# Performance work log

Measured on AMD Instinct MI355X. Metric: run time of the kernel, lower is better.

The kernel has to match this reference:

```python
import jax, jax.numpy as jnp
import numpy as np

N_USER = 100000
N_ITEM = 50000
N = N_USER + N_ITEM
EMB = 64
FEAT = 384
NNZ = 2400000
N_PROMPT = 8
N_LAYERS = 4
EPS = 1e-8


def setup_inputs() -> dict:
    key = jax.random.key(0)
    ks = jax.random.split(key, 8)
    user_fea = jax.random.normal(ks[0], (N_USER, EMB), jnp.float32)
    item_fea = jax.random.normal(ks[1], (N_ITEM, FEAT), jnp.float32)
    prompt_embedding = jax.random.normal(ks[2], (N_PROMPT, EMB), jnp.float32)
    mlp_w = jax.random.normal(ks[3], (FEAT, EMB), jnp.float32) / np.sqrt(FEAT)
    mlp_b = jnp.zeros((EMB,), jnp.float32)
    adj_rows = jax.random.randint(ks[4], (NNZ,), 0, N, jnp.int32)
    adj_cols = jax.random.randint(ks[5], (NNZ,), 0, N, jnp.int32)
    # normalized-adjacency-like positive values
    adj_vals = jax.random.uniform(ks[6], (NNZ,), jnp.float32) * 0.01
    return dict(user_fea=user_fea, item_fea=item_fea,
                prompt_embedding=prompt_embedding, mlp_w=mlp_w, mlp_b=mlp_b,
                adj_rows=adj_rows, adj_cols=adj_cols, adj_vals=adj_vals)


def _spmm(rows, cols, vals, x):
    # sparse [N,N] @ dense [N,E] via gather + segment-sum
    return jax.ops.segment_sum(vals[:, None] * x[cols], rows, num_segments=N)


def reference(user_fea, item_fea, prompt_embedding, mlp_w, mlp_b,
              adj_rows, adj_cols, adj_vals):
    prompt_embd = jnp.sum(prompt_embedding, axis=0)            # [EMB]
    user_embd = user_fea + prompt_embd[None, :]                # [N_USER, EMB]
    item_embd = jnp.tanh(item_fea @ mlp_w + mlp_b)             # [N_ITEM, EMB]
    ego = jnp.concatenate([user_embd, item_embd], axis=0)      # [N, EMB]
    ego_norm = jnp.linalg.norm(ego, axis=-1)                   # [N]

    x = ego
    acc = ego  # running sum over layer stack (layer 0 = ego)
    for _ in range(N_LAYERS):
        x = _spmm(adj_rows, adj_cols, adj_vals, x)
        # cosine similarity of propagated embedding vs ego embedding, per row
        denom = jnp.maximum(jnp.linalg.norm(x, axis=-1) * ego_norm, EPS)
        w = jnp.sum(x * ego, axis=-1) / denom                  # [N]
        x = w[:, None] * x
        acc = acc + x

    return acc[:N_USER], acc[N_USER:]
```

## Files before the change

kernel.cpp:

```cpp
#include <hip/hip_runtime.h>
#include <hip/hip_fp16.h>

constexpr int kNUser = 100000;
constexpr int kNItem = 50000;
constexpr int kN     = 150000;
constexpr int kEmb   = 64;
constexpr int kFeat  = 384;
constexpr int kNnz   = 2400000;
constexpr float kEps = 1e-8f;

constexpr int kChunk = 1024;
constexpr int kNB    = (kN + kChunk - 1) / kChunk;

constexpr int kNBkt   = 256;
constexpr int kBR     = (kN + kNBkt - 1) / kNBkt;
constexpr int kChunkA = 4096;
constexpr int kNWGA   = (kNnz + kChunkA - 1) / kChunkA;

constexpr int kKS     = kFeat / 32;
constexpr int kNT     = kEmb / 16;
constexpr int kWElems = kKS * kNT * 64 * 8;

typedef __attribute__((ext_vector_type(8))) short short8v;
typedef __attribute__((ext_vector_type(4))) float floatx4;

__device__ inline unsigned short f2bf(float f) {
    unsigned u = __float_as_uint(f);
    return (unsigned short)((u + 0x7FFFu + ((u >> 16) & 1u)) >> 16);
}
__device__ inline float bf2f(unsigned short h) {
    return __uint_as_float((unsigned)h << 16);
}


__global__ void prompt_sum_k(const float* __restrict__ p, float* __restrict__ out) {
    int d = threadIdx.x;
    float s = 0.f;
#pragma unroll
    for (int i = 0; i < 8; ++i) s += p[i * kEmb + d];
    out[d] = s;
}

__global__ void user_ego_k(const float* __restrict__ uf, const float* __restrict__ ps,
                           float* __restrict__ ego) {
    int i = blockIdx.x * blockDim.x + threadIdx.x;
    if (i >= kNUser * kEmb) return;
    ego[i] = uf[i] + ps[i & 63];
}

__global__ void wsplit_k(const float* __restrict__ w, unsigned short* __restrict__ whi,
                         unsigned short* __restrict__ wlo) {
    int t = blockIdx.x * 256 + threadIdx.x;
    if (t >= kWElems) return;
    int j    = t & 7;
    int lane = (t >> 3) & 63;
    int nt   = (t >> 9) & 3;
    int ks   = t >> 11;
    int k = ks * 32 + (lane >> 4) * 8 + j;
    int n = nt * 16 + (lane & 15);
    float v = w[k * kEmb + n];
    unsigned short h = f2bf(v);
    whi[t] = h;
    wlo[t] = f2bf(v - bf2f(h));
}

__global__ __launch_bounds__(256)
void item_ego_mfma_k(const float* __restrict__ itf, const unsigned short* __restrict__ whi,
                     const unsigned short* __restrict__ wlo, const float* __restrict__ b,
                     float* __restrict__ ego) {
    int t    = threadIdx.x;
    int wid  = t >> 6;
    int lane = t & 63;
    int r0   = blockIdx.x * 64 + wid * 16;
    int arow = r0 + (lane & 15);
    int kg   = lane >> 4;
    bool av  = arow < kNItem;
    const float* ap = itf + (size_t)(av ? arow : 0) * kFeat + kg * 8;

    const short8v* whv = (const short8v*)whi;
    const short8v* wlv = (const short8v*)wlo;

    floatx4 accH[kNT], accL[kNT];
#pragma unroll
    for (int nt = 0; nt < kNT; ++nt) {
        accH[nt] = (floatx4){0.f, 0.f, 0.f, 0.f};
        accL[nt] = (floatx4){0.f, 0.f, 0.f, 0.f};
    }

    for (int ks = 0; ks < kKS; ++ks) {
        const float4 z = make_float4(0.f, 0.f, 0.f, 0.f);
        float4 a0 = av ? *(const float4*)(ap + ks * 32)     : z;
        float4 a1 = av ? *(const float4*)(ap + ks * 32 + 4) : z;
        short8v ah, al;
#pragma unroll
        for (int j = 0; j < 8; ++j) {
            float f = (j < 4) ? ((const float*)&a0)[j] : ((const float*)&a1)[j - 4];
            unsigned short h = f2bf(f);
            ah[j] = (short)h;
            al[j] = (short)f2bf(f - bf2f(h));
        }
#pragma unroll
        for (int nt = 0; nt < kNT; ++nt) {
            short8v bh = whv[(ks * kNT + nt) * 64 + lane];
            short8v bl = wlv[(ks * kNT + nt) * 64 + lane];
            accH[nt] = __builtin_amdgcn_mfma_f32_16x16x32_bf16(ah, bh, accH[nt], 0, 0, 0);
            accL[nt] = __builtin_amdgcn_mfma_f32_16x16x32_bf16(ah, bl, accL[nt], 0, 0, 0);
            accL[nt] = __builtin_amdgcn_mfma_f32_16x16x32_bf16(al, bh, accL[nt], 0, 0, 0);
        }
    }

    int col0  = lane & 15;
    int rsub  = (lane >> 4) * 4;
#pragma unroll
    for (int nt = 0; nt < kNT; ++nt) {
        float bb = b[nt * 16 + col0];
#pragma unroll
        for (int r = 0; r < 4; ++r) {
            int row = r0 + rsub + r;
            if (row < kNItem)
                ego[(size_t)(kNUser + row) * kEmb + nt * 16 + col0] =
                    tanhf(accH[nt][r] + accL[nt][r] + bb);
        }
    }
}

constexpr int kRW      = 16;
constexpr int kRowsBlk = 64;
constexpr int kKc      = 32;

__global__ __launch_bounds__(256, 2)
void item_ego_k(const float* __restrict__ itf, const float* __restrict__ w,
                const float* __restrict__ b, float* __restrict__ ego) {
    __shared__ float lds_a[kRowsBlk * kKc];
    int t      = threadIdx.x;
    int wid    = t >> 6;
    int lane   = t & 63;
    int blk_r0 = blockIdx.x * kRowsBlk;

    float acc[kRW];
#pragma unroll
    for (int r = 0; r < kRW; ++r) acc[r] = 0.f;

    int srow = t >> 3;
    int scol = (t & 7) * 4;

    for (int kc = 0; kc < kFeat; kc += kKc) {
        __syncthreads();
        {
            const float4 z = make_float4(0.f, 0.f, 0.f, 0.f);
            int gr0 = blk_r0 + srow;
            int gr1 = gr0 + 32;
            float4 v0 = (gr0 < kNItem)
                ? *(const float4*)(itf + (size_t)gr0 * kFeat + kc + scol) : z;
            float4 v1 = (gr1 < kNItem)
                ? *(const float4*)(itf + (size_t)gr1 * kFeat + kc + scol) : z;
            *(float4*)(lds_a + srow * kKc + scol)        = v0;
            *(float4*)(lds_a + (srow + 32) * kKc + scol) = v1;
        }
        float wreg[kKc];
#pragma unroll
        for (int k = 0; k < kKc; ++k) wreg[k] = w[(kc + k) * kEmb + lane];
        __syncthreads();
#pragma unroll
        for (int r = 0; r < kRW; ++r) {
            const float4* av = (const float4*)(lds_a + (wid * kRW + r) * kKc);
#pragma unroll
            for (int q = 0; q < 8; ++q) {
                float4 a = av[q];
                acc[r] = fmaf(a.x, wreg[q * 4 + 0], acc[r]);
                acc[r] = fmaf(a.y, wreg[q * 4 + 1], acc[r]);
                acc[r] = fmaf(a.z, wreg[q * 4 + 2], acc[r]);
                acc[r] = fmaf(a.w, wreg[q * 4 + 3], acc[r]);
            }
        }
    }
    float bv = b[lane];
#pragma unroll
    for (int r = 0; r < kRW; ++r) {
        int row = blk_r0 + wid * kRW + r;
        if (row < kNItem)
            ego[(size_t)(kNUser + row) * kEmb + lane] = tanhf(acc[r] + bv);
    }
}

__global__ void norm_init_csr_k(const float* __restrict__ ego, float* __restrict__ nrm,
                                float* __restrict__ acc, unsigned short* __restrict__ egoh) {
    int wid  = threadIdx.x >> 6;
    int lane = threadIdx.x & 63;
    int row  = blockIdx.x * 4 + wid;
    if (row >= kN) return;
    size_t idx = (size_t)row * kEmb + lane;
    float e = ego[idx];
    acc[idx] = e;
    __half h = __float2half_rn(e);
    egoh[idx] = *(unsigned short*)&h;
    float s = e * e;
#pragma unroll
    for (int o = 32; o >= 1; o >>= 1) s += __shfl_xor(s, o, 64);
    if (lane == 0) nrm[row] = sqrtf(s);
}


__global__ void hist_k(const int* __restrict__ rows, int* __restrict__ cnt) {
    int e = blockIdx.x * blockDim.x + threadIdx.x;
    if (e < kNnz) atomicAdd(&cnt[rows[e]], 1);
}

__global__ void scan1_k(const int* __restrict__ cnt, int* __restrict__ excl_out,
                        int* __restrict__ blk_sum) {
    __shared__ int sd[256];
    int b = blockIdx.x, t = threadIdx.x;
    int base = b * kChunk + t * 4;
    int c0 = (base + 0 < kN) ? cnt[base + 0] : 0;
    int c1 = (base + 1 < kN) ? cnt[base + 1] : 0;
    int c2 = (base + 2 < kN) ? cnt[base + 2] : 0;
    int c3 = (base + 3 < kN) ? cnt[base + 3] : 0;
    int tsum = c0 + c1 + c2 + c3;
    sd[t] = tsum;
    __syncthreads();
#pragma unroll
    for (int off = 1; off < 256; off <<= 1) {
        int v = (t >= off) ? sd[t - off] : 0;
        __syncthreads();
        sd[t] += v;
        __syncthreads();
    }
    int excl = sd[t] - tsum;
    if (t == 255) blk_sum[b] = sd[255];
    int run = excl;
    if (base + 0 < kN) { excl_out[base + 0] = run; run += c0; }
    if (base + 1 < kN) { excl_out[base + 1] = run; run += c1; }
    if (base + 2 < kN) { excl_out[base + 2] = run; run += c2; }
    if (base + 3 < kN) { excl_out[base + 3] = run; run += c3; }
}

__global__ void scan2_k(const int* __restrict__ blk_sum, int* __restrict__ blk_off) {
    __shared__ int sd[256];
    int t = threadIdx.x;
    int v = (t < kNB) ? blk_sum[t] : 0;
    sd[t] = v;
    __syncthreads();
#pragma unroll
    for (int off = 1; off < 256; off <<= 1) {
        int u = (t >= off) ? sd[t - off] : 0;
        __syncthreads();
        sd[t] += u;
        __syncthreads();
    }
    if (t < kNB) blk_off[t] = sd[t] - v;
}

__global__ void scan3_k(int* __restrict__ rp, int* __restrict__ rf,
                        const int* __restrict__ blk_off) {
    int b = blockIdx.x, t = threadIdx.x;
    int base = b * kChunk + t * 4;
    int o = blk_off[b];
#pragma unroll
    for (int k = 0; k < 4; ++k) {
        int i = base + k;
        if (i < kN) { int v = rp[i] + o; rp[i] = v; rf[i] = v; }
    }
    if (b == 0 && t == 0) rp[kN] = kNnz;
}

__global__ void bbase_k(const int* __restrict__ rp, int* __restrict__ bbase) {
    int b = blockIdx.x * blockDim.x + threadIdx.x;
    if (b <= kNBkt) {
        int r = b * kBR;
        bbase[b] = rp[r < kN ? r : kN];
    }
}

__global__ __launch_bounds__(256)
void bucket_k(const int* __restrict__ rows, const int* __restrict__ cols,
              const float* __restrict__ vals, const int* __restrict__ bbase,
              int* __restrict__ bfill, int2* __restrict__ tmp) {
    __shared__ int cnt[kNBkt];
    __shared__ int wgbase[kNBkt];
    int t  = threadIdx.x;
    int e0 = blockIdx.x * kChunkA;
    for (int i = t; i < kNBkt; i += 256) cnt[i] = 0;
    __syncthreads();
    int myb[kChunkA / 256];
    int myoff[kChunkA / 256];
#pragma unroll
    for (int k = 0; k < kChunkA / 256; ++k) {
        int e = e0 + k * 256 + t;
        if (e < kNnz) {
            int b = rows[e] / kBR;
            myb[k]   = b;
            myoff[k] = atomicAdd(&cnt[b], 1);
        } else {
            myb[k] = -1;
        }
    }
    __syncthreads();
    for (int i = t; i < kNBkt; i += 256)
        wgbase[i] = cnt[i] ? atomicAdd(&bfill[i], cnt[i]) : 0;
    __syncthreads();
#pragma unroll
    for (int k = 0; k < kChunkA / 256; ++k) {
        int b = myb[k];
        if (b < 0) continue;
        int e = e0 + k * 256 + t;
        int pos = bbase[b] + wgbase[b] + myoff[k];
        int rowrel = rows[e] - b * kBR;
        tmp[pos] = make_int2((rowrel << 18) | cols[e], __float_as_int(vals[e]));
    }
}

__global__ __launch_bounds__(256)
void debucket_k(const int2* __restrict__ tmp, const int* __restrict__ bbase,
                int* __restrict__ rf, int2* __restrict__ csr) {
    int b  = blockIdx.x;
    int t  = threadIdx.x;
    int j0 = bbase[b];
    int j1 = bbase[b + 1];
    int rbase = b * kBR;
    for (int jb = j0; jb < j1; jb += 1024) {
        int2 e[4];
        int  pos[4];
        bool v[4];
#pragma unroll
        for (int q = 0; q < 4; ++q) {
            int j = jb + q * 256 + t;
            v[q] = j < j1;
            if (v[q]) e[q] = tmp[j];
        }
#pragma unroll
        for (int q = 0; q < 4; ++q)
            if (v[q]) {
                int row = rbase + (int)((unsigned)e[q].x >> 18);
                pos[q] = atomicAdd(&rf[row], 1);
            }
#pragma unroll
        for (int q = 0; q < 4; ++q)
            if (v[q]) csr[pos[q]] = make_int2(e[q].x & 0x3FFFF, e[q].y);
    }
}

__global__ __launch_bounds__(256)
void layer_k(const int* __restrict__ rp, const int2* __restrict__ csr,
             const float* __restrict__ ego, const float* __restrict__ nrm,
             const unsigned short* __restrict__ xin_h,
             unsigned short* __restrict__ xout_h,
             float* __restrict__ acc, int write_x) {
    int wid  = threadIdx.x >> 6;
    int lane = threadIdx.x & 63;
    int row  = blockIdx.x * 4 + wid;
    if (row >= kN) return;
    int q   = lane >> 4;
    int sub = lane & 15;
    int p0 = rp[row];
    int p1 = rp[row + 1];

    float4 s = make_float4(0.f, 0.f, 0.f, 0.f);
    for (int base = p0; base < p1; base += 16) {
        int2  e[4];
        float w[4];
#pragma unroll
        for (int g = 0; g < 4; ++g) {
            int j  = base + g * 4 + q;
            bool v = j < p1;
            e[g] = csr[v ? j : p0];
            w[g] = v ? __int_as_float(e[g].y) : 0.f;
        }
        uint2 gv[4];
#pragma unroll
        for (int g = 0; g < 4; ++g)
            gv[g] = *(const uint2*)(xin_h + (size_t)e[g].x * kEmb + sub * 4);
#pragma unroll
        for (int g = 0; g < 4; ++g) {
            float2 f0 = __half22float2(*(const __half2*)&gv[g].x);
            float2 f1 = __half22float2(*(const __half2*)&gv[g].y);
            s.x = fmaf(w[g], f0.x, s.x);
            s.y = fmaf(w[g], f0.y, s.y);
            s.z = fmaf(w[g], f1.x, s.z);
            s.w = fmaf(w[g], f1.y, s.w);
        }
    }
#pragma unroll
    for (int o = 16; o <= 32; o <<= 1) {
        s.x += __shfl_xor(s.x, o, 64);
        s.y += __shfl_xor(s.y, o, 64);
        s.z += __shfl_xor(s.z, o, 64);
        s.w += __shfl_xor(s.w, o, 64);
    }
    size_t idx = (size_t)row * kEmb + sub * 4;
    const float4 ev = *(const float4*)(ego + idx);
    float d = s.x * ev.x + s.y * ev.y + s.z * ev.z + s.w * ev.w;
    float n = s.x * s.x + s.y * s.y + s.z * s.z + s.w * s.w;
#pragma unroll
    for (int o = 1; o <= 8; o <<= 1) {
        d += __shfl_xor(d, o, 64);
        n += __shfl_xor(n, o, 64);
    }
    float wgt = d / fmaxf(sqrtf(n) * nrm[row], kEps);
    if (q == 0) {
        float4 xw = make_float4(wgt * s.x, wgt * s.y, wgt * s.z, wgt * s.w);
        if (write_x) {
            __half2 o0 = __floats2half2_rn(xw.x, xw.y);
            __half2 o1 = __floats2half2_rn(xw.z, xw.w);
            uint2 st;
            st.x = *(unsigned*)&o0;
            st.y = *(unsigned*)&o1;
            *(uint2*)(xout_h + idx) = st;
        }
        float4 av = *(const float4*)(acc + idx);
        av.x += xw.x; av.y += xw.y; av.z += xw.z; av.w += xw.w;
        *(float4*)(acc + idx) = av;
    }
}


__global__ void norm_init_full_k(const float* __restrict__ ego, float* __restrict__ nrm,
                                 float* __restrict__ x, float* __restrict__ acc) {
    int wid  = threadIdx.x >> 6;
    int lane = threadIdx.x & 63;
    int row  = blockIdx.x * 4 + wid;
    if (row >= kN) return;
    size_t idx = (size_t)row * kEmb + lane;
    float e = ego[idx];
    x[idx]   = e;
    acc[idx] = e;
    float s = e * e;
#pragma unroll
    for (int o = 32; o >= 1; o >>= 1) s += __shfl_xor(s, o, 64);
    if (lane == 0) nrm[row] = sqrtf(s);
}

__global__ void spmm_k(const int* __restrict__ rows, const int* __restrict__ cols,
                       const float* __restrict__ vals, const float* __restrict__ x,
                       float* __restrict__ y) {
    long long t = (long long)blockIdx.x * blockDim.x + threadIdx.x;
    int e = (int)(t >> 6);
    if (e >= kNnz) return;
    int lane = threadIdx.x & 63;
    atomicAdd(y + (size_t)rows[e] * kEmb + lane, vals[e] * x[(size_t)cols[e] * kEmb + lane]);
}

__global__ void weight_k(const float* __restrict__ ego, const float* __restrict__ nrm,
                         const float* __restrict__ y, float* __restrict__ x,
                         float* __restrict__ acc) {
    int wid  = threadIdx.x >> 6;
    int lane = threadIdx.x & 63;
    int row  = blockIdx.x * 4 + wid;
    if (row >= kN) return;
    size_t idx = (size_t)row * kEmb + lane;
    float yv = y[idx];
    float ev = ego[idx];
    float d = yv * ev;
    float n = yv * yv;
#pragma unroll
    for (int o = 32; o >= 1; o >>= 1) {
        d += __shfl_xor(d, o, 64);
        n += __shfl_xor(n, o, 64);
    }
    float w  = d / fmaxf(sqrtf(n) * nrm[row], kEps);
    float xw = w * yv;
    x[idx] = xw;
    acc[idx] += xw;
}


extern "C" void kernel_launch(void* const* d_in, const int* in_sizes, int n_in,
                              void* d_out, int out_size, void* d_ws, size_t ws_size,
                              hipStream_t stream) {
    const float* user_fea = (const float*)d_in[0];
    const float* item_fea = (const float*)d_in[1];
    const float* prompt   = (const float*)d_in[2];
    const float* mlp_w    = (const float*)d_in[3];
    const float* mlp_b    = (const float*)d_in[4];
    const int*   adj_rows = (const int*)d_in[5];
    const int*   adj_cols = (const int*)d_in[6];
    const float* adj_vals = (const float*)d_in[7];
    float* acc = (float*)d_out;

    const size_t NE = (size_t)kN * kEmb;
    float* ws = (float*)d_ws;

    size_t off = 0;
    float* f_ego = ws + off; off += NE;
    float* f_ps  = ws + off; off += 64;
    float* f_nrm = ws + off; off += kN;
    size_t branch0 = off;
    unsigned short* f_egoh = (unsigned short*)(ws + off); off += NE / 2;
    unsigned short* f_xha  = (unsigned short*)(ws + off); off += NE / 2;
    unsigned short* f_xhb  = (unsigned short*)(ws + off); off += NE / 2;
    int* row_cnt  = (int*)(ws + off); off += kN;
    int* row_ptr  = (int*)(ws + off); off += kN + 1;
    int* row_fill = (int*)(ws + off); off += kN;
    int* blk_sum  = (int*)(ws + off); off += kNB;
    int* blk_off  = (int*)(ws + off); off += kNB;
    int* bbase    = (int*)(ws + off); off += kNBkt + 1;
    int* bfill    = (int*)(ws + off); off += kNBkt;
    off = (off + 3) & ~(size_t)3;
    unsigned short* whi = (unsigned short*)(ws + off); off += kWElems / 2;
    unsigned short* wlo = (unsigned short*)(ws + off); off += kWElems / 2;
    off = (off + 1) & ~(size_t)1;
    int2* csr = (int2*)(ws + off); off += (size_t)kNnz * 2;
    const bool use_csr = ws_size >= off * 4;

    prompt_sum_k<<<1, 64, 0, stream>>>(prompt, f_ps);
    user_ego_k<<<(kNUser * kEmb + 255) / 256, 256, 0, stream>>>(user_fea, f_ps, f_ego);

    if (use_csr) {
        wsplit_k<<<(kWElems + 255) / 256, 256, 0, stream>>>(mlp_w, whi, wlo);
        item_ego_mfma_k<<<(kNItem + 63) / 64, 256, 0, stream>>>(item_fea, whi, wlo,
                                                                mlp_b, f_ego);

        int2* tmp = (int2*)f_xha;
        hipMemsetAsync(row_cnt, 0, kN * sizeof(int), stream);
        hipMemsetAsync(bfill, 0, kNBkt * sizeof(int), stream);
        hist_k<<<(kNnz + 255) / 256, 256, 0, stream>>>(adj_rows, row_cnt);
        scan1_k<<<kNB, 256, 0, stream>>>(row_cnt, row_ptr, blk_sum);
        scan2_k<<<1, 256, 0, stream>>>(blk_sum, blk_off);
        scan3_k<<<kNB, 256, 0, stream>>>(row_ptr, row_fill, blk_off);
        bbase_k<<<2, 256, 0, stream>>>(row_ptr, bbase);
        bucket_k<<<kNWGA, 256, 0, stream>>>(adj_rows, adj_cols, adj_vals,
                                            bbase, bfill, tmp);
        debucket_k<<<kNBkt, 256, 0, stream>>>(tmp, bbase, row_fill, csr);

        norm_init_csr_k<<<(kN + 3) / 4, 256, 0, stream>>>(f_ego, f_nrm, acc, f_egoh);

        const unsigned short* xin = f_egoh;
        unsigned short* xout = f_xha;
        for (int l = 0; l < 4; ++l) {
            layer_k<<<(kN + 3) / 4, 256, 0, stream>>>(row_ptr, csr, f_ego, f_nrm,
                                                      xin, xout, acc, (l < 3) ? 1 : 0);
            xin  = xout;
            xout = (xout == f_xha) ? f_xhb : f_xha;
        }
    } else {
        float* f_x = ws + branch0;
        float* f_y = f_x + NE;
        item_ego_k<<<(kNItem + kRowsBlk - 1) / kRowsBlk, 256, 0, stream>>>(
            item_fea, mlp_w, mlp_b, f_ego);
        norm_init_full_k<<<(kN + 3) / 4, 256, 0, stream>>>(f_ego, f_nrm, f_x, acc);
        for (int l = 0; l < 4; ++l) {
            hipMemsetAsync(f_y, 0, NE * sizeof(float), stream);
            spmm_k<<<(int)(((long long)kNnz * 64 + 255) / 256), 256, 0, stream>>>(
                adj_rows, adj_cols, adj_vals, f_x, f_y);
            weight_k<<<(kN + 3) / 4, 256, 0, stream>>>(f_ego, f_nrm, f_y, f_x, acc);
        }
    }
}
```

Before: 857.7 us.

## Build CSR via bucket-local scans and defer accumulation to final layer

Replaces the global per-row histogram plus three-pass scan with a per-bucket count, a single small bucket scan, and a debucket kernel that computes row pointers and places entries using shared-memory atomics instead of global ones. Keeps all three intermediate half-precision layer outputs and sums them with ego in the last layer, so the fp32 acc array is read and written once instead of on every layer and no longer initialised separately. This removes several launches and much global traffic in exchange for an extra workspace buffer and a final sum of fp16-rounded layer outputs, which could differ slightly in precision.

```diff
diff --git a/kernel.cpp b/kernel.cpp
--- a/kernel.cpp
+++ b/kernel.cpp
@@ -8,9 +8,6 @@
 constexpr int kFeat  = 384;
 constexpr int kNnz   = 2400000;
 constexpr float kEps = 1e-8f;
-
-constexpr int kChunk = 1024;
-constexpr int kNB    = (kN + kChunk - 1) / kChunk;
 
 constexpr int kNBkt   = 256;
 constexpr int kBR     = (kN + kNBkt - 1) / kNBkt;
@@ -184,14 +181,13 @@
 }
 
 __global__ void norm_init_csr_k(const float* __restrict__ ego, float* __restrict__ nrm,
-                                float* __restrict__ acc, unsigned short* __restrict__ egoh) {
+                                unsigned short* __restrict__ egoh) {
     int wid  = threadIdx.x >> 6;
     int lane = threadIdx.x & 63;
     int row  = blockIdx.x * 4 + wid;
     if (row >= kN) return;
     size_t idx = (size_t)row * kEmb + lane;
     float e = ego[idx];
-    acc[idx] = e;
     __half h = __float2half_rn(e);
     egoh[idx] = *(unsigned short*)&h;
     float s = e * e;
@@ -201,74 +197,40 @@
 }
 
 
-__global__ void hist_k(const int* __restrict__ rows, int* __restrict__ cnt) {
-    int e = blockIdx.x * blockDim.x + threadIdx.x;
-    if (e < kNnz) atomicAdd(&cnt[rows[e]], 1);
-}
-
-__global__ void scan1_k(const int* __restrict__ cnt, int* __restrict__ excl_out,
-                        int* __restrict__ blk_sum) {
-    __shared__ int sd[256];
-    int b = blockIdx.x, t = threadIdx.x;
-    int base = b * kChunk + t * 4;
-    int c0 = (base + 0 < kN) ? cnt[base + 0] : 0;
-    int c1 = (base + 1 < kN) ? cnt[base + 1] : 0;
-    int c2 = (base + 2 < kN) ? cnt[base + 2] : 0;
-    int c3 = (base + 3 < kN) ? cnt[base + 3] : 0;
-    int tsum = c0 + c1 + c2 + c3;
-    sd[t] = tsum;
-    __syncthreads();
-#pragma unroll
-    for (int off = 1; off < 256; off <<= 1) {
-        int v = (t >= off) ? sd[t - off] : 0;
-        __syncthreads();
-        sd[t] += v;
-        __syncthreads();
-    }
-    int excl = sd[t] - tsum;
-    if (t == 255) blk_sum[b] = sd[255];
-    int run = excl;
-    if (base + 0 < kN) { excl_out[base + 0] = run; run += c0; }
-    if (base + 1 < kN) { excl_out[base + 1] = run; run += c1; }
-    if (base + 2 < kN) { excl_out[base + 2] = run; run += c2; }
-    if (base + 3 < kN) { excl_out[base + 3] = run; run += c3; }
-}
-
-__global__ void scan2_k(const int* __restrict__ blk_sum, int* __restrict__ blk_off) {
-    __shared__ int sd[256];
+__global__ __launch_bounds__(256)
+void bcnt_k(const int* __restrict__ rows, int* __restrict__ bcnt) {
+    __shared__ int cnt[kNBkt];
+    int t  = threadIdx.x;
+    int e0 = blockIdx.x * kChunkA;
+    for (int i = t; i < kNBkt; i += 256) cnt[i] = 0;
+    __syncthreads();
+#pragma unroll
+    for (int k = 0; k < kChunkA / 256; ++k) {
+        int e = e0 + k * 256 + t;
+        if (e < kNnz) atomicAdd(&cnt[rows[e] / kBR], 1);
+    }
+    __syncthreads();
+    for (int i = t; i < kNBkt; i += 256)
+        if (cnt[i]) atomicAdd(&bcnt[i], cnt[i]);
+}
+
+__global__ void bscan_k(const int* __restrict__ bcnt, int* __restrict__ bbase,
+                        int* __restrict__ bfill) {
+    __shared__ int sd[kNBkt];
     int t = threadIdx.x;
-    int v = (t < kNB) ? blk_sum[t] : 0;
+    int v = bcnt[t];
     sd[t] = v;
     __syncthreads();
 #pragma unroll
-    for (int off = 1; off < 256; off <<= 1) {
+    for (int off = 1; off < kNBkt; off <<= 1) {
         int u = (t >= off) ? sd[t - off] : 0;
         __syncthreads();
         sd[t] += u;
         __syncthreads();
     }
-    if (t < kNB) blk_off[t] = sd[t] - v;
-}
-
-__global__ void scan3_k(int* __restrict__ rp, int* __restrict__ rf,
-                        const int* __restrict__ blk_off) {
-    int b = blockIdx.x, t = threadIdx.x;
-    int base = b * kChunk + t * 4;
-    int o = blk_off[b];
-#pragma unroll
-    for (int k = 0; k < 4; ++k) {
-        int i = base + k;
-        if (i < kN) { int v = rp[i] + o; rp[i] = v; rf[i] = v; }
-    }
-    if (b == 0 && t == 0) rp[kN] = kNnz;
-}
-
-__global__ void bbase_k(const int* __restrict__ rp, int* __restrict__ bbase) {
-    int b = blockIdx.x * blockDim.x + threadIdx.x;
-    if (b <= kNBkt) {
-        int r = b * kBR;
-        bbase[b] = rp[r < kN ? r : kN];
-    }
+    bbase[t] = sd[t] - v;
+    if (t == kNBkt - 1) bbase[kNBkt] = kNnz;
+    bfill[t] = 0;
 }
 
 __global__ __launch_bounds__(256)
@@ -310,32 +272,52 @@
 }
 
 __global__ __launch_bounds__(256)
-void debucket_k(const int2* __restrict__ tmp, const int* __restrict__ bbase,
-                int* __restrict__ rf, int2* __restrict__ csr) {
+void debucket2_k(const int2* __restrict__ tmp, const int* __restrict__ bbase,
+                 int* __restrict__ rp, int2* __restrict__ csr) {
+    __shared__ int rcnt[kBR];
+    __shared__ int rbaseL[kBR];
+    __shared__ int sd[256];
     int b  = blockIdx.x;
     int t  = threadIdx.x;
     int j0 = bbase[b];
     int j1 = bbase[b + 1];
-    int rbase = b * kBR;
-    for (int jb = j0; jb < j1; jb += 1024) {
-        int2 e[4];
-        int  pos[4];
-        bool v[4];
-#pragma unroll
-        for (int q = 0; q < 4; ++q) {
-            int j = jb + q * 256 + t;
-            v[q] = j < j1;
-            if (v[q]) e[q] = tmp[j];
-        }
-#pragma unroll
-        for (int q = 0; q < 4; ++q)
-            if (v[q]) {
-                int row = rbase + (int)((unsigned)e[q].x >> 18);
-                pos[q] = atomicAdd(&rf[row], 1);
-            }
-#pragma unroll
-        for (int q = 0; q < 4; ++q)
-            if (v[q]) csr[pos[q]] = make_int2(e[q].x & 0x3FFFF, e[q].y);
+    for (int i = t; i < kBR; i += 256) rcnt[i] = 0;
+    __syncthreads();
+    for (int j = j0 + t; j < j1; j += 256)
+        atomicAdd(&rcnt[(unsigned)tmp[j].x >> 18], 1);
+    __syncthreads();
+    int base = t * 3;
+    int c0 = (base     < kBR) ? rcnt[base]     : 0;
+    int c1 = (base + 1 < kBR) ? rcnt[base + 1] : 0;
+    int c2 = (base + 2 < kBR) ? rcnt[base + 2] : 0;
+    int tsum = c0 + c1 + c2;
+    sd[t] = tsum;
+    __syncthreads();
+#pragma unroll
+    for (int off = 1; off < 256; off <<= 1) {
+        int u = (t >= off) ? sd[t - off] : 0;
+        __syncthreads();
+        sd[t] += u;
+        __syncthreads();
+    }
+    int g0 = j0 + sd[t] - tsum;
+    if (base     < kBR) rbaseL[base]     = g0;
+    if (base + 1 < kBR) rbaseL[base + 1] = g0 + c0;
+    if (base + 2 < kBR) rbaseL[base + 2] = g0 + c0 + c1;
+    __syncthreads();
+    int rbaseG = b * kBR;
+    for (int i = t; i < kBR; i += 256) {
+        int r = rbaseG + i;
+        if (r < kN) rp[r] = rbaseL[i];
+    }
+    if (b == kNBkt - 1 && t == 0) rp[kN] = kNnz;
+    for (int i = t; i < kBR; i += 256) rcnt[i] = 0;
+    __syncthreads();
+    for (int j = j0 + t; j < j1; j += 256) {
+        int2 e = tmp[j];
+        int rr = (unsigned)e.x >> 18;
+        int pos = rbaseL[rr] + atomicAdd(&rcnt[rr], 1);
+        csr[pos] = make_int2(e.x & 0x3FFFF, e.y);
     }
 }
 
@@ -344,7 +326,9 @@
              const float* __restrict__ ego, const float* __restrict__ nrm,
              const unsigned short* __restrict__ xin_h,
              unsigned short* __restrict__ xout_h,
-             float* __restrict__ acc, int write_x) {
+             const unsigned short* __restrict__ xh1,
+             const unsigned short* __restrict__ xh2,
+             float* __restrict__ acc, int last) {
     int wid  = threadIdx.x >> 6;
     int lane = threadIdx.x & 63;
     int row  = blockIdx.x * 4 + wid;
@@ -398,17 +382,30 @@
     float wgt = d / fmaxf(sqrtf(n) * nrm[row], kEps);
     if (q == 0) {
         float4 xw = make_float4(wgt * s.x, wgt * s.y, wgt * s.z, wgt * s.w);
-        if (write_x) {
+        if (!last) {
             __half2 o0 = __floats2half2_rn(xw.x, xw.y);
             __half2 o1 = __floats2half2_rn(xw.z, xw.w);
             uint2 st;
             st.x = *(unsigned*)&o0;
             st.y = *(unsigned*)&o1;
             *(uint2*)(xout_h + idx) = st;
-        }
-        float4 av = *(const float4*)(acc + idx);
-        av.x += xw.x; av.y += xw.y; av.z += xw.z; av.w += xw.w;
-        *(float4*)(acc + idx) = av;
+        } else {
+            uint2 a1 = *(const uint2*)(xh1 + idx);
+            uint2 a2 = *(const uint2*)(xh2 + idx);
+            uint2 a3 = *(const uint2*)(xin_h + idx);
+            float2 f1a = __half22float2(*(const __half2*)&a1.x);
+            float2 f1b = __half22float2(*(const __half2*)&a1.y);
+            float2 f2a = __half22float2(*(const __half2*)&a2.x);
+            float2 f2b = __half22float2(*(const __half2*)&a2.y);
+            float2 f3a = __half22float2(*(const __half2*)&a3.x);
+            float2 f3b = __half22float2(*(const __half2*)&a3.y);
+            float4 out;
+            out.x = ev.x + f1a.x + f2a.x + f3a.x + xw.x;
+            out.y = ev.y + f1a.y + f2a.y + f3a.y + xw.y;
+            out.z = ev.z + f1b.x + f2b.x + f3b.x + xw.z;
+            out.w = ev.w + f1b.y + f2b.y + f3b.y + xw.w;
+            *(float4*)(acc + idx) = out;
+        }
     }
 }
 
@@ -485,15 +482,13 @@
     float* f_nrm = ws + off; off += kN;
     size_t branch0 = off;
     unsigned short* f_egoh = (unsigned short*)(ws + off); off += NE / 2;
-    unsigned short* f_xha  = (unsigned short*)(ws + off); off += NE / 2;
-    unsigned short* f_xhb  = (unsigned short*)(ws + off); off += NE / 2;
-    int* row_cnt  = (int*)(ws + off); off += kN;
-    int* row_ptr  = (int*)(ws + off); off += kN + 1;
-    int* row_fill = (int*)(ws + off); off += kN;
-    int* blk_sum  = (int*)(ws + off); off += kNB;
-    int* blk_off  = (int*)(ws + off); off += kNB;
-    int* bbase    = (int*)(ws + off); off += kNBkt + 1;
-    int* bfill    = (int*)(ws + off); off += kNBkt;
+    unsigned short* f_xh1  = (unsigned short*)(ws + off); off += NE / 2;
+    unsigned short* f_xh2  = (unsigned short*)(ws + off); off += NE / 2;
+    unsigned short* f_xh3  = (unsigned short*)(ws + off); off += NE / 2;
+    int* row_ptr = (int*)(ws + off); off += kN + 1;
+    int* bcnt    = (int*)(ws + off); off += kNBkt;
+    int* bbase   = (int*)(ws + off); off += kNBkt + 1;
+    int* bfill   = (int*)(ws + off); off += kNBkt;
     off = (off + 3) & ~(size_t)3;
     unsigned short* whi = (unsigned short*)(ws + off); off += kWElems / 2;
     unsigned short* wlo = (unsigned short*)(ws + off); off += kWElems / 2;
@@ -509,28 +504,28 @@
         item_ego_mfma_k<<<(kNItem + 63) / 64, 256, 0, stream>>>(item_fea, whi, wlo,
                                                                 mlp_b, f_ego);
 
-        int2* tmp = (int2*)f_xha;
-        hipMemsetAsync(row_cnt, 0, kN * sizeof(int), stream);
-        hipMemsetAsync(bfill, 0, kNBkt * sizeof(int), stream);
-        hist_k<<<(kNnz + 255) / 256, 256, 0, stream>>>(adj_rows, row_cnt);
-        scan1_k<<<kNB, 256, 0, stream>>>(row_cnt, row_ptr, blk_sum);
-        scan2_k<<<1, 256, 0, stream>>>(blk_sum, blk_off);
-        scan3_k<<<kNB, 256, 0, stream>>>(row_ptr, row_fill, blk_off);
-        bbase_k<<<2, 256, 0, stream>>>(row_ptr, bbase);
+        int2* tmp = (int2*)f_xh1;
+        hipMemsetAsync(bcnt, 0, kNBkt * sizeof(int), stream);
+        bcnt_k<<<kNWGA, 256, 0, stream>>>(adj_rows, bcnt);
+        bscan_k<<<1, kNBkt, 0, stream>>>(bcnt, bbase, bfill);
         bucket_k<<<kNWGA, 256, 0, stream>>>(adj_rows, adj_cols, adj_vals,
                                             bbase, bfill, tmp);
-        debucket_k<<<kNBkt, 256, 0, stream>>>(tmp, bbase, row_fill, csr);
-
-        norm_init_csr_k<<<(kN + 3) / 4, 256, 0, stream>>>(f_ego, f_nrm, acc, f_egoh);
-
-        const unsigned short* xin = f_egoh;
-        unsigned short* xout = f_xha;
-        for (int l = 0; l < 4; ++l) {
-            layer_k<<<(kN + 3) / 4, 256, 0, stream>>>(row_ptr, csr, f_ego, f_nrm,
-                                                      xin, xout, acc, (l < 3) ? 1 : 0);
-            xin  = xout;
-            xout = (xout == f_xha) ? f_xhb : f_xha;
-        }
+        debucket2_k<<<kNBkt, 256, 0, stream>>>(tmp, bbase, row_ptr, csr);
+
+        norm_init_csr_k<<<(kN + 3) / 4, 256, 0, stream>>>(f_ego, f_nrm, f_egoh);
+
+        layer_k<<<(kN + 3) / 4, 256, 0, stream>>>(row_ptr, csr, f_ego, f_nrm,
+                                                  f_egoh, f_xh1, nullptr, nullptr,
+                                                  acc, 0);
+        layer_k<<<(kN + 3) / 4, 256, 0, stream>>>(row_ptr, csr, f_ego, f_nrm,
+                                                  f_xh1, f_xh2, nullptr, nullptr,
+                                                  acc, 0);
+        layer_k<<<(kN + 3) / 4, 256, 0, stream>>>(row_ptr, csr, f_ego, f_nrm,
+                                                  f_xh2, f_xh3, nullptr, nullptr,
+                                                  acc, 0);
+        layer_k<<<(kN + 3) / 4, 256, 0, stream>>>(row_ptr, csr, f_ego, f_nrm,
+                                                  f_xh3, nullptr, f_xh1, f_xh2,
+                                                  acc, 1);
     } else {
         float* f_x = ws + branch0;
         float* f_y = f_x + NE;
```

Measured after the change: 711.1 us. 17.1% less time.
